# Optimization experiments

Hardware: AMD Instinct MI355X
Metric: run time of the kernel (lower is better)

The kernel has to match this reference:

```python
import jax, jax.numpy as jnp
import numpy as np

B, T, F, U, M = 4096, 16, 256, 512, 8
DELTA_T = 0.04

# ln_tau_table: tau = 1, 10^0.5, 10^1.0, ... -> ln(tau) = i * 0.5*ln(10)
LN_TAU = (jnp.arange(M, dtype=jnp.float32) * (0.5 * np.log(10.0))).astype(jnp.float32)
DECAY = jnp.exp(-DELTA_T / (LN_TAU + 1e-7))  # [M]


def setup_inputs() -> dict:
    key = jax.random.key(0)
    ks = jax.random.split(key, 9)
    s = lambda fan_in: 1.0 / np.sqrt(fan_in)
    return {
        "x": jax.random.normal(ks[0], (B, T, F), dtype=jnp.float32),
        "W_r": jax.random.normal(ks[1], (F + U, U * M), dtype=jnp.float32) * s(F + U),
        "b_r": jax.random.normal(ks[2], (U * M,), dtype=jnp.float32) * 0.01,
        "W_q": jax.random.normal(ks[3], (F + U, U), dtype=jnp.float32) * s(F + U),
        "b_q": jax.random.normal(ks[4], (U,), dtype=jnp.float32) * 0.01,
        "W_s": jax.random.normal(ks[5], (F + U, U * M), dtype=jnp.float32) * s(F + U),
        "b_s": jax.random.normal(ks[6], (U * M,), dtype=jnp.float32) * 0.01,
        "W_out": jax.random.normal(ks[7], (U, 3), dtype=jnp.float32) * s(U),
        "b_out": jax.random.normal(ks[8], (3,), dtype=jnp.float32) * 0.01,
    }


def _ctgru_forward(x, W_r, b_r, W_q, b_q, W_s, b_s, W_out, b_out):
    def step(h_hat, x_t):  # h_hat: [B,U,M], x_t: [B,F]
        h = h_hat.sum(axis=2)                              # [B,U]
        fused = jnp.concatenate([x_t, h], axis=1)          # [B,F+U]
        ln_tau_r = (fused @ W_r + b_r).reshape(-1, U, M)   # [B,U,M]
        r_ki = jax.nn.softmax(-jnp.square(ln_tau_r - LN_TAU), axis=2)
        q_in = jnp.concatenate([x_t, jnp.sum(r_ki * h_hat, axis=2)], axis=1)
        q_k = jnp.tanh(q_in @ W_q + b_q)[:, :, None]       # [B,U,1]
        ln_tau_s = (fused @ W_s + b_s).reshape(-1, U, M)
        s_ki = jax.nn.softmax(-jnp.square(ln_tau_s - LN_TAU), axis=2)
        h_next = ((1.0 - s_ki) * h_hat + s_ki * q_k) * DECAY
        return h_next, h_next.sum(axis=2)                  # carry, hidden [B,U]

    h0 = jnp.zeros((x.shape[0], U, M), dtype=x.dtype)
    _, hiddens = jax.lax.scan(step, h0, jnp.swapaxes(x, 0, 1))  # hiddens: [T,B,U]
    outputs = jnp.swapaxes(hiddens, 0, 1)                  # [B,T,U]
    return outputs @ W_out + b_out                         # [B,T,3]


def reference(x, W_r, b_r, W_q, b_q, W_s, b_s, W_out, b_out):
    return _ctgru_forward(x, W_r, b_r, W_q, b_q, W_s, b_s, W_out, b_out)
```

## Files before the change

### kernel.cpp

```cpp
#include <hip/hip_runtime.h>
#include <hip/hip_bf16.h>
#include <math.h>

#define B_   4096
#define T_   16
#define F_   256
#define U_   512
#define M_   8
#define K_   768
#define NRS  4096
#define NC   8192
#define LNT  1.1512925f

typedef __bf16 bf16_t;
typedef bf16_t bf16x8 __attribute__((ext_vector_type(8)));
typedef bf16_t bf16x4 __attribute__((ext_vector_type(4)));
typedef float  f32x4  __attribute__((ext_vector_type(4)));

__device__ inline void gl_lds16(const void* g, void* lds) {
    __builtin_amdgcn_global_load_lds(
        (const __attribute__((address_space(1))) unsigned int*)g,
        (__attribute__((address_space(3))) unsigned int*)lds, 16, 0, 0);
}

#define VMCNT(n) asm volatile("s_waitcnt vmcnt(" #n ")" ::: "memory")
#define LGKM0()  asm volatile("s_waitcnt lgkmcnt(0)" ::: "memory")
#define BAR()    __builtin_amdgcn_s_barrier()

__device__ inline void stage_slot(const bf16_t* src, bf16_t* dst, int tid) {
    gl_lds16(src + tid * 8,        (char*)dst + tid * 16);
    gl_lds16(src + tid * 8 + 4096, (char*)dst + tid * 16 + 8192);
}

__device__ inline void ds_read4(const bf16_t* base, bf16x8 (&v)[4]) {
    v[0] = *(const bf16x8*)(base);
    v[1] = *(const bf16x8*)(base + 512);
    v[2] = *(const bf16x8*)(base + 1024);
    v[3] = *(const bf16x8*)(base + 1536);
}

template <int H>
__device__ inline void mfma16(f32x4 (&acc)[8][4], const bf16x8 (&a)[4],
                              const bf16x8 (&b)[4]) {
    __builtin_amdgcn_s_setprio(1);
#pragma unroll
    for (int i = 0; i < 4; ++i)
#pragma unroll
        for (int j = 0; j < 4; ++j)
            acc[H * 4 + i][j] = __builtin_amdgcn_mfma_f32_16x16x32_bf16(
                a[i], b[j], acc[H * 4 + i][j], 0, 0, 0);
    __builtin_amdgcn_s_setprio(0);
}

__global__ __launch_bounds__(512, 2) void gemm_rs_tp(
    const bf16_t* __restrict__ xt_t,
    const bf16_t* __restrict__ ht,
    const bf16_t* __restrict__ Bt,
    const float*  __restrict__ biasP,
    const bf16_t* __restrict__ hhat,
    bf16_t* __restrict__ rh,
    bf16_t* __restrict__ sbuf)
{
    __shared__ __attribute__((aligned(16))) bf16_t Asl[2][8192];
    __shared__ __attribute__((aligned(16))) bf16_t Bsl[2][8192];

    const int tid  = threadIdx.x;
    const int lane = tid & 63;
    const int wave = tid >> 6;

    const int lin = blockIdx.y * 16 + blockIdx.x;
    const int xcd = lin & 7, q = lin >> 3;
    const int m0 = ((xcd >> 1) * 4 + (q & 3)) * 256;
    const int n0 = ((xcd & 1) * 16 + (q >> 2)) * 256;
    const int mp = m0 >> 8, np = n0 >> 8;

    const int wm = wave >> 2;
    const int wn = wave & 3;
    const int lr = lane & 15;
    const int kq = lane >> 4;
    const int cr = (kq ^ ((lr >> 1) & 3)) * 8;

    const int aoff0 = (wm * 128 + lr) * 32 + cr;
    const int aoff1 = (wm * 128 + 64 + lr) * 32 + cr;
    const int boff  = (wn * 64 + lr) * 32 + cr;

    f32x4 acc[8][4] = {};
    bf16x8 a[4], b[4];

#define ASRC(S) ((S) < 8 ? xt_t + (size_t)(mp * 8 + (S)) * 8192               \
                         : ht   + (size_t)(mp * 16 + (S) - 8) * 8192)
#define BSRC(S) (Bt + (size_t)(np * 24 + (S)) * 8192)

    stage_slot(ASRC(0), &Asl[0][0], tid);
    stage_slot(BSRC(0), &Bsl[0][0], tid);
    VMCNT(0);
    BAR();

#define TILE(T, SFLAG)                                                        \
  {                                                                           \
    const int p_ = (T) & 1, pn_ = p_ ^ 1;                                     \
    if (SFLAG) {                                                              \
      stage_slot(ASRC((T) + 1), &Asl[pn_][0], tid);                           \
      stage_slot(BSRC((T) + 1), &Bsl[pn_][0], tid);                           \
    }                                                                         \
    ds_read4(&Asl[p_][0] + aoff0, a);                                         \
    ds_read4(&Bsl[p_][0] + boff, b);                                          \
    LGKM0();                                                                  \
    mfma16<0>(acc, a, b);                                                     \
    ds_read4(&Asl[p_][0] + aoff1, a);                                         \
    LGKM0();                                                                  \
    mfma16<1>(acc, a, b);                                                     \
    VMCNT(0);                                                                 \
    BAR();                                                                    \
  }

    for (int tt = 0; tt < 22; tt += 2) { TILE(tt, 1); TILE(tt + 1, 1); }
    TILE(22, 1);
    TILE(23, 0);
#undef TILE
#undef ASRC
#undef BSRC

    const int nb  = n0 + wn * 64;
    const int u3  = lane & 7;
    const int m0v = ((lane >> 3) & 1) * 4;
    const bool is_r = nb < NRS;

    float bj[4];
#pragma unroll
    for (int j = 0; j < 4; ++j) bj[j] = biasP[nb + j * 16 + lr];

#pragma unroll
    for (int mi = 0; mi < 8; ++mi) {
        const int rowb = m0 + wm * 128 + mi * 16 + kq * 4;
#pragma unroll
        for (int r = 0; r < 4; ++r) {
            const int row = rowb + r;
            float e[4], sum = 0.f;
#pragma unroll
            for (int j = 0; j < 4; ++j) {
                float v = acc[mi][j][r] + bj[j];
                float d = v - (float)(m0v + j) * LNT;
                e[j] = __expf(-d * d);
                sum += e[j];
            }
            sum += __shfl_xor(sum, 8, 64);
            const float inv = 1.0f / sum;
            if (is_r) {
                bf16x4 h4 = *(const bf16x4*)(hhat + (size_t)row * NRS + nb + u3 * 8 + m0v);
                float rhv = 0.f;
#pragma unroll
                for (int j = 0; j < 4; ++j) rhv += e[j] * inv * (float)h4[j];
                rhv += __shfl_xor(rhv, 8, 64);
                if ((lane & 8) == 0)
                    rh[(size_t)row * U_ + (nb >> 3) + u3] = (bf16_t)rhv;
            } else {
                bf16x4 pv;
#pragma unroll
                for (int j = 0; j < 4; ++j) pv[j] = (bf16_t)(e[j] * inv);
                *(bf16x4*)(sbuf + (size_t)row * NRS + (nb - NRS) + u3 * 8 + m0v) = pv;
            }
        }
    }
}

__global__ __launch_bounds__(256) void gemm_q_up(
    const bf16_t* __restrict__ xt_t,
    const bf16_t* __restrict__ rh,
    const bf16_t* __restrict__ Bq,
    const float*  __restrict__ bq,
    const bf16_t* __restrict__ sbuf,
    bf16_t* __restrict__ hhat,
    bf16_t* __restrict__ hnext,
    bf16_t* __restrict__ htile)
{
    __shared__ __attribute__((aligned(16))) bf16_t Al[2][64 * 32];
    __shared__ __attribute__((aligned(16))) bf16_t Bl[2][64 * 32];

    const int tid  = threadIdx.x;
    const int lane = tid & 63;
    const int wave = tid >> 6;
    const int m0 = blockIdx.x * 64;
    const int n0 = blockIdx.y * 64;
    const int wm = (wave & 1) * 32;
    const int wn = (wave >> 1) * 32;
    const int lr = lane & 15;
    const int kq = lane >> 4;
    const int crq = (kq ^ ((lr >> 1) & 3)) * 8;

    f32x4 acc[2][2] = {};

    const int rA  = tid >> 2;
    const int kc  = (tid & 3) * 8;
    const int kcs = ((tid & 3) ^ ((tid >> 3) & 3)) * 8;

    for (int kk = 0; kk < K_; kk += 64) {
        __syncthreads();
        if (kk < F_) {
            const bf16_t* s0p = xt_t + (size_t)((m0 >> 8) * 8 + (kk >> 5)) * 8192
                                     + (size_t)(m0 & 255) * 32;
            gl_lds16(s0p + tid * 8,        (char*)&Al[0][0] + tid * 16);
            gl_lds16(s0p + 8192 + tid * 8, (char*)&Al[1][0] + tid * 16);
        } else {
            const int cb = kk - F_;
            gl_lds16(rh + (size_t)(m0 + rA) * U_ + cb + kcs,      (char*)&Al[0][0] + tid * 16);
            gl_lds16(rh + (size_t)(m0 + rA) * U_ + cb + 32 + kcs, (char*)&Al[1][0] + tid * 16);
        }
        gl_lds16(Bq + (size_t)(n0 + rA) * K_ + kk + kc,      (char*)&Bl[0][0] + tid * 16);
        gl_lds16(Bq + (size_t)(n0 + rA) * K_ + kk + 32 + kc, (char*)&Bl[1][0] + tid * 16);
        __syncthreads();

#pragma unroll
        for (int s = 0; s < 2; s++) {
            bf16x8 af[2], bfr[2];
#pragma unroll
            for (int i = 0; i < 2; i++)
                af[i] = *(const bf16x8*)(&Al[s][0] + (wm + i * 16 + lr) * 32 + crq);
#pragma unroll
            for (int i = 0; i < 2; i++)
                bfr[i] = *(const bf16x8*)(&Bl[s][0] + (wn + i * 16 + lr) * 32 + kq * 8);
#pragma unroll
            for (int i = 0; i < 2; i++)
#pragma unroll
                for (int j = 0; j < 2; j++)
                    acc[i][j] = __builtin_amdgcn_mfma_f32_16x16x32_bf16(
                        af[i], bfr[j], acc[i][j], 0, 0, 0);
        }
    }

    const float DEC[8] = {0.0f, 0.9658531f, 0.9827783f, 0.9884856f,
                          0.9913518f, 0.9930754f, 0.9942261f, 0.9950489f};

#pragma unroll
    for (int i = 0; i < 2; i++) {
        const int rowb = m0 + wm + i * 16 + kq * 4;
#pragma unroll
        for (int j = 0; j < 2; j++) {
            const int u = n0 + wn + j * 16 + lr;
            const float bv = bq[u];
            const int us = u >> 5, uc = u & 31;
#pragma unroll
            for (int r = 0; r < 4; r++) {
                const int row = rowb + r;
                const float q = tanhf(acc[i][j][r] + bv);
                const size_t base = (size_t)row * NRS + u * 8;
                bf16x8 s8 = *(const bf16x8*)(sbuf + base);
                bf16x8 h8 = *(const bf16x8*)(hhat + base);
                bf16x8 ho;
                float hs = 0.f;
#pragma unroll
                for (int m = 0; m < 8; m++) {
                    float s = (float)s8[m];
                    float h = (float)h8[m];
                    float hn = ((1.f - s) * h + s * q) * DEC[m];
                    ho[m] = (bf16_t)hn;
                    hs += hn;
                }
                *(bf16x8*)(hhat + base) = ho;
                hnext[(size_t)row * U_ + u] = (bf16_t)hs;
                const int rl = row & 255;
                htile[(size_t)((row >> 8) * 16 + us) * 8192 + rl * 32
                      + (((uc >> 3) ^ ((rl >> 1) & 3)) * 8) + (uc & 7)] = (bf16_t)hs;
            }
        }
    }
}

__global__ void transpose_perm(const float* __restrict__ src, bf16_t* __restrict__ dst) {
    __shared__ float tl[32][33];
    int k0 = blockIdx.x * 32, n0 = blockIdx.y * 32;
    int tx = threadIdx.x & 31, ty = threadIdx.x >> 5;
#pragma unroll
    for (int i = 0; i < 32; i += 8)
        tl[ty + i][tx] = src[(size_t)(k0 + ty + i) * NRS + n0 + tx];
    __syncthreads();
#pragma unroll
    for (int i = 0; i < 32; i += 8) {
        int n = n0 + ty + i;
        int m = n & 7, u3v = (n >> 3) & 7;
        int p = (n & ~63) + (m & 3) * 16 + (m >> 2) * 8 + u3v;
        dst[(size_t)p * K_ + k0 + tx] = (bf16_t)tl[tx][ty + i];
    }
}

__global__ void btile_build(const bf16_t* __restrict__ WrsT, bf16_t* __restrict__ Bt) {
    int n = blockIdx.x / 3;
    int k = (blockIdx.x % 3) * 256 + threadIdx.x;
    int p = n >> 8, r = n & 255, s = k >> 5, c = k & 31;
    Bt[(size_t)(p * 24 + s) * 8192 + r * 32
       + (((c >> 3) ^ ((r >> 1) & 3)) * 8) + (c & 7)] = WrsT[(size_t)n * K_ + k];
}

__global__ void transpose_plain(const float* __restrict__ src, bf16_t* __restrict__ dst, int N) {
    __shared__ float tl[32][33];
    int k0 = blockIdx.x * 32, n0 = blockIdx.y * 32;
    int tx = threadIdx.x & 31, ty = threadIdx.x >> 5;
#pragma unroll
    for (int i = 0; i < 32; i += 8)
        tl[ty + i][tx] = src[(size_t)(k0 + ty + i) * N + n0 + tx];
    __syncthreads();
#pragma unroll
    for (int i = 0; i < 32; i += 8)
        dst[(size_t)(n0 + ty + i) * K_ + k0 + tx] = (bf16_t)tl[tx][ty + i];
}

__global__ void bias_perm(const float* __restrict__ b_r, const float* __restrict__ b_s,
                          float* __restrict__ biasP) {
    int p = blockIdx.x * 256 + threadIdx.x;
    int pr = p & 63, j = pr >> 4, lr = pr & 15;
    int L = (p & ~63) + (lr & 7) * 8 + ((lr >> 3) & 1) * 4 + j;
    biasP[p] = (L < NRS) ? b_r[L] : b_s[L - NRS];
}

__global__ void xtile_build(const float* __restrict__ x, bf16_t* __restrict__ xt) {
    int idx = blockIdx.x * 256 + threadIdx.x;
    int b = idx >> 12;
    int rem = idx & 4095;
    int t = rem >> 8, f = rem & 255;
    int mp = b >> 8, r = b & 255, s = f >> 5, c = f & 31;
    xt[((size_t)(t * 16 + mp) * 8 + s) * 8192 + r * 32
       + (((c >> 3) ^ ((r >> 1) & 3)) * 8) + (c & 7)] = (bf16_t)x[idx];
}

__global__ __launch_bounds__(256) void out_all(
    const bf16_t* __restrict__ hall,
    const float* __restrict__ Wout,
    const float* __restrict__ bout,
    float* __restrict__ out)
{
    int row = blockIdx.x * 4 + (threadIdx.x >> 6);
    int lane = threadIdx.x & 63;
    bf16x8 h8 = *(const bf16x8*)(hall + (size_t)row * U_ + lane * 8);
    float p0 = 0, p1 = 0, p2 = 0;
#pragma unroll
    for (int k = 0; k < 8; k++) {
        float h = (float)h8[k];
        int u = lane * 8 + k;
        p0 += h * Wout[u * 3 + 0];
        p1 += h * Wout[u * 3 + 1];
        p2 += h * Wout[u * 3 + 2];
    }
    for (int off = 32; off; off >>= 1) {
        p0 += __shfl_down(p0, off, 64);
        p1 += __shfl_down(p1, off, 64);
        p2 += __shfl_down(p2, off, 64);
    }
    if (lane == 0) {
        int t = row >> 12, b = row & (B_ - 1);
        size_t o = ((size_t)b * T_ + t) * 3;
        out[o + 0] = p0 + bout[0];
        out[o + 1] = p1 + bout[1];
        out[o + 2] = p2 + bout[2];
    }
}

extern "C" void kernel_launch(void* const* d_in, const int* in_sizes, int n_in,
                              void* d_out, int out_size, void* d_ws, size_t ws_size,
                              hipStream_t stream) {
    const float* x   = (const float*)d_in[0];
    const float* W_r = (const float*)d_in[1];
    const float* b_r = (const float*)d_in[2];
    const float* W_q = (const float*)d_in[3];
    const float* b_q = (const float*)d_in[4];
    const float* W_s = (const float*)d_in[5];
    const float* b_s = (const float*)d_in[6];
    const float* W_o = (const float*)d_in[7];
    const float* b_o = (const float*)d_in[8];
    float* out = (float*)d_out;

    char* ws = (char*)d_ws;
    bf16_t* hhat  = (bf16_t*)ws; ws += (size_t)B_ * NRS * 2;
    bf16_t* sbuf  = (bf16_t*)ws; ws += (size_t)B_ * NRS * 2;
    bf16_t* xtile = (bf16_t*)ws; ws += (size_t)B_ * T_ * F_ * 2;
    bf16_t* hall  = (bf16_t*)ws; ws += (size_t)(T_ + 1) * B_ * U_ * 2;
    bf16_t* rh    = (bf16_t*)ws; ws += (size_t)B_ * U_ * 2;
    bf16_t* WrsT  = (bf16_t*)ws; ws += (size_t)NC * K_ * 2;
    bf16_t* Btile = (bf16_t*)ws; ws += (size_t)NC * K_ * 2;
    bf16_t* htile = (bf16_t*)ws; ws += (size_t)B_ * U_ * 2;
    bf16_t* WqT   = (bf16_t*)ws; ws += (size_t)U_ * K_ * 2;
    float*  biasP = (float*)ws;  ws += (size_t)NC * 4;

    hipMemsetAsync(hhat, 0, (size_t)B_ * NRS * 2, stream);
    hipMemsetAsync(htile, 0, (size_t)B_ * U_ * 2, stream);
    xtile_build<<<B_ * T_ * F_ / 256, 256, 0, stream>>>(x, xtile);
    transpose_perm<<<dim3(K_ / 32, NRS / 32), 256, 0, stream>>>(W_r, WrsT);
    transpose_perm<<<dim3(K_ / 32, NRS / 32), 256, 0, stream>>>(W_s, WrsT + (size_t)NRS * K_);
    btile_build<<<NC * 3, 256, 0, stream>>>(WrsT, Btile);
    transpose_plain<<<dim3(K_ / 32, U_ / 32), 256, 0, stream>>>(W_q, WqT, U_);
    bias_perm<<<NC / 256, 256, 0, stream>>>(b_r, b_s, biasP);

    for (int t = 0; t < T_; t++) {
        const bf16_t* xt_t = xtile + (size_t)t * 16 * 8 * 8192;
        bf16_t*       hn   = hall + (size_t)(t + 1) * B_ * U_;
        gemm_rs_tp<<<dim3(16, 32), 512, 0, stream>>>(xt_t, htile, Btile, biasP, hhat, rh, sbuf);
        gemm_q_up<<<dim3(64, 8), 256, 0, stream>>>(xt_t, rh, WqT, b_q, sbuf, hhat, hn, htile);
    }
    out_all<<<B_ * T_ / 4, 256, 0, stream>>>(hall + (size_t)B_ * U_, W_o, b_o, out);
}
```

Before: 1.792 ms.

## Restructure rs GEMM to K=64 tiles with 8-phase interleaved LDS pipeline

The main r/s GEMM now stages 64-wide K tiles split into halves and double-buffers them across two slots. Each iteration runs an 8-phase schedule that interleaves LDS reads, global-to-LDS loads and MFMA quarters, with barriers between phases. The swizzled tile layouts for x, h, W_rs and a new pre-tiled W_q are rewritten to a 64-column XOR swizzle, so the q GEMM can load B directly from tiles. LDS use rises to 128KB, so occupancy drops to one block per CU, and the many barriers add sync cost in exchange for better overlap of loads with MFMA.

```diff
diff --git a/kernel.cpp b/kernel.cpp
--- a/kernel.cpp
+++ b/kernel.cpp
@@ -27,32 +27,12 @@
 #define LGKM0()  asm volatile("s_waitcnt lgkmcnt(0)" ::: "memory")
 #define BAR()    __builtin_amdgcn_s_barrier()
 
-__device__ inline void stage_slot(const bf16_t* src, bf16_t* dst, int tid) {
+__device__ inline void stage_ht(const bf16_t* src, bf16_t* dst, int tid) {
     gl_lds16(src + tid * 8,        (char*)dst + tid * 16);
     gl_lds16(src + tid * 8 + 4096, (char*)dst + tid * 16 + 8192);
 }
 
-__device__ inline void ds_read4(const bf16_t* base, bf16x8 (&v)[4]) {
-    v[0] = *(const bf16x8*)(base);
-    v[1] = *(const bf16x8*)(base + 512);
-    v[2] = *(const bf16x8*)(base + 1024);
-    v[3] = *(const bf16x8*)(base + 1536);
-}
-
-template <int H>
-__device__ inline void mfma16(f32x4 (&acc)[8][4], const bf16x8 (&a)[4],
-                              const bf16x8 (&b)[4]) {
-    __builtin_amdgcn_s_setprio(1);
-#pragma unroll
-    for (int i = 0; i < 4; ++i)
-#pragma unroll
-        for (int j = 0; j < 4; ++j)
-            acc[H * 4 + i][j] = __builtin_amdgcn_mfma_f32_16x16x32_bf16(
-                a[i], b[j], acc[H * 4 + i][j], 0, 0, 0);
-    __builtin_amdgcn_s_setprio(0);
-}
-
-__global__ __launch_bounds__(512, 2) void gemm_rs_tp(
+__global__ __launch_bounds__(512, 1) void gemm_rs_v8(
     const bf16_t* __restrict__ xt_t,
     const bf16_t* __restrict__ ht,
     const bf16_t* __restrict__ Bt,
@@ -61,8 +41,8 @@
     bf16_t* __restrict__ rh,
     bf16_t* __restrict__ sbuf)
 {
-    __shared__ __attribute__((aligned(16))) bf16_t Asl[2][8192];
-    __shared__ __attribute__((aligned(16))) bf16_t Bsl[2][8192];
+    __shared__ __attribute__((aligned(16))) bf16_t Ah[2][2][8192];
+    __shared__ __attribute__((aligned(16))) bf16_t Bh[2][2][8192];
 
     const int tid  = threadIdx.x;
     const int lane = tid & 63;
@@ -78,57 +58,107 @@
     const int wn = wave & 3;
     const int lr = lane & 15;
     const int kq = lane >> 4;
-    const int cr = (kq ^ ((lr >> 1) & 3)) * 8;
-
-    const int aoff0 = (wm * 128 + lr) * 32 + cr;
-    const int aoff1 = (wm * 128 + 64 + lr) * 32 + cr;
-    const int boff  = (wn * 64 + lr) * 32 + cr;
+    const int ck0 = (kq ^ (lr & 7)) * 8;
+
+    const bf16_t* Ab0 = &Ah[0][wm][0] + lr * 64;
+    const bf16_t* Ab1 = &Ah[1][wm][0] + lr * 64;
+    const bf16_t* Bb0 = &Bh[0][wn >> 1][0] + ((wn & 1) * 64 + lr) * 64;
+    const bf16_t* Bb1 = &Bh[1][wn >> 1][0] + ((wn & 1) * 64 + lr) * 64;
 
     f32x4 acc[8][4] = {};
-    bf16x8 a[4], b[4];
-
-#define ASRC(S) ((S) < 8 ? xt_t + (size_t)(mp * 8 + (S)) * 8192               \
-                         : ht   + (size_t)(mp * 16 + (S) - 8) * 8192)
-#define BSRC(S) (Bt + (size_t)(np * 24 + (S)) * 8192)
-
-    stage_slot(ASRC(0), &Asl[0][0], tid);
-    stage_slot(BSRC(0), &Bsl[0][0], tid);
-    VMCNT(0);
+    bf16x8 a[8], b[8];
+
+#define AS(T, H) ((T) < 4 ? xt_t + ((size_t)(mp * 4 + (T)) * 2 + (H)) * 8192  \
+                          : ht  + ((size_t)(mp * 8 + (T) - 4) * 2 + (H)) * 8192)
+#define BS(T, H) (Bt + ((size_t)(np * 12 + (T)) * 2 + (H)) * 8192)
+
+#define RDA(P, mh) do{ const bf16_t* _p = (P) + (mh) * 4096;                   \
+    a[0]=*(const bf16x8*)(_p+ck0);      a[1]=*(const bf16x8*)(_p+(ck0^32));    \
+    a[2]=*(const bf16x8*)(_p+1024+ck0); a[3]=*(const bf16x8*)(_p+1024+(ck0^32)); \
+    a[4]=*(const bf16x8*)(_p+2048+ck0); a[5]=*(const bf16x8*)(_p+2048+(ck0^32)); \
+    a[6]=*(const bf16x8*)(_p+3072+ck0); a[7]=*(const bf16x8*)(_p+3072+(ck0^32)); }while(0)
+
+#define RDB(P, nh) do{ const bf16_t* _p = (P) + (nh) * 2048;                   \
+    b[(nh)*4+0]=*(const bf16x8*)(_p+ck0);                                      \
+    b[(nh)*4+1]=*(const bf16x8*)(_p+(ck0^32));                                 \
+    b[(nh)*4+2]=*(const bf16x8*)(_p+1024+ck0);                                 \
+    b[(nh)*4+3]=*(const bf16x8*)(_p+1024+(ck0^32)); }while(0)
+
+#define MMA(MH, NH) do{ __builtin_amdgcn_s_setprio(1);                         \
+    _Pragma("unroll") for (int ai = 0; ai < 4; ++ai)                           \
+      _Pragma("unroll") for (int bj = 0; bj < 2; ++bj)                         \
+        acc[(MH)*4+ai][(NH)*2+bj] = __builtin_amdgcn_mfma_f32_16x16x32_bf16(   \
+            a[ai*2+0], b[(NH)*4+bj*2+0], acc[(MH)*4+ai][(NH)*2+bj], 0, 0, 0);  \
+    _Pragma("unroll") for (int ai = 0; ai < 4; ++ai)                           \
+      _Pragma("unroll") for (int bj = 0; bj < 2; ++bj)                         \
+        acc[(MH)*4+ai][(NH)*2+bj] = __builtin_amdgcn_mfma_f32_16x16x32_bf16(   \
+            a[ai*2+1], b[(NH)*4+bj*2+1], acc[(MH)*4+ai][(NH)*2+bj], 0, 0, 0);  \
+    __builtin_amdgcn_s_setprio(0); }while(0)
+
+    stage_ht(AS(0, 0), &Ah[0][0][0], tid);
+    stage_ht(AS(0, 1), &Ah[0][1][0], tid);
+    stage_ht(BS(0, 0), &Bh[0][0][0], tid);
+    stage_ht(BS(0, 1), &Bh[0][1][0], tid);
+    stage_ht(AS(1, 0), &Ah[1][0][0], tid);
+    stage_ht(AS(1, 1), &Ah[1][1][0], tid);
+    stage_ht(BS(1, 0), &Bh[1][0][0], tid);
+    stage_ht(BS(1, 1), &Bh[1][1][0], tid);
+    VMCNT(8);
     BAR();
 
-#define TILE(T, SFLAG)                                                        \
-  {                                                                           \
-    const int p_ = (T) & 1, pn_ = p_ ^ 1;                                     \
-    if (SFLAG) {                                                              \
-      stage_slot(ASRC((T) + 1), &Asl[pn_][0], tid);                           \
-      stage_slot(BSRC((T) + 1), &Bsl[pn_][0], tid);                           \
-    }                                                                         \
-    ds_read4(&Asl[p_][0] + aoff0, a);                                         \
-    ds_read4(&Bsl[p_][0] + boff, b);                                          \
-    LGKM0();                                                                  \
-    mfma16<0>(acc, a, b);                                                     \
-    ds_read4(&Asl[p_][0] + aoff1, a);                                         \
-    LGKM0();                                                                  \
-    mfma16<1>(acc, a, b);                                                     \
-    VMCNT(0);                                                                 \
-    BAR();                                                                    \
-  }
-
-    for (int tt = 0; tt < 22; tt += 2) { TILE(tt, 1); TILE(tt + 1, 1); }
-    TILE(22, 1);
-    TILE(23, 0);
-#undef TILE
-#undef ASRC
-#undef BSRC
+#define ITER_S(E) do{                                                          \
+    RDA(Ab0,0); RDB(Bb0,0);                    BAR(); LGKM0(); MMA(0,0); BAR();\
+    RDB(Bb0,1);                                BAR(); LGKM0(); MMA(0,1); BAR();\
+    RDA(Ab0,1); stage_ht(BS((E)+2,0), &Bh[0][0][0], tid);                      \
+                                               BAR(); LGKM0(); MMA(1,1); BAR();\
+    stage_ht(BS((E)+2,1), &Bh[0][1][0], tid);                                  \
+                                    BAR(); LGKM0(); MMA(1,0); VMCNT(4); BAR(); \
+    RDA(Ab1,0); RDB(Bb1,0); stage_ht(AS((E)+2,0), &Ah[0][0][0], tid);          \
+                                               BAR(); LGKM0(); MMA(0,0); BAR();\
+    RDB(Bb1,1); stage_ht(AS((E)+2,1), &Ah[0][1][0], tid);                      \
+                                               BAR(); LGKM0(); MMA(0,1); BAR();\
+    RDA(Ab1,1); stage_ht(BS((E)+3,0), &Bh[1][0][0], tid);                      \
+                                               BAR(); LGKM0(); MMA(1,1); BAR();\
+    stage_ht(BS((E)+3,1), &Bh[1][1][0], tid);                                  \
+    stage_ht(AS((E)+3,0), &Ah[1][0][0], tid);                                  \
+    stage_ht(AS((E)+3,1), &Ah[1][1][0], tid);                                  \
+                                    BAR(); LGKM0(); MMA(1,0); VMCNT(8); BAR(); \
+}while(0)
+
+#define ITER_L() do{                                                           \
+    RDA(Ab0,0); RDB(Bb0,0);                    BAR(); LGKM0(); MMA(0,0); BAR();\
+    RDB(Bb0,1);                                BAR(); LGKM0(); MMA(0,1); BAR();\
+    RDA(Ab0,1);                                BAR(); LGKM0(); MMA(1,1); BAR();\
+                                    BAR(); LGKM0(); MMA(1,0); VMCNT(0); BAR(); \
+    RDA(Ab1,0); RDB(Bb1,0);                    BAR(); LGKM0(); MMA(0,0); BAR();\
+    RDB(Bb1,1);                                BAR(); LGKM0(); MMA(0,1); BAR();\
+    RDA(Ab1,1);                                BAR(); LGKM0(); MMA(1,1); BAR();\
+                                               BAR(); LGKM0(); MMA(1,0);       \
+}while(0)
+
+    ITER_S(0);
+    ITER_S(2);
+    ITER_S(4);
+    ITER_S(6);
+    ITER_S(8);
+    ITER_L();
+
+#undef ITER_S
+#undef ITER_L
+#undef MMA
+#undef RDA
+#undef RDB
+#undef AS
+#undef BS
 
     const int nb  = n0 + wn * 64;
     const int u3  = lane & 7;
     const int m0v = ((lane >> 3) & 1) * 4;
     const bool is_r = nb < NRS;
 
-    float bj[4];
-#pragma unroll
-    for (int j = 0; j < 4; ++j) bj[j] = biasP[nb + j * 16 + lr];
+    float bj4[4];
+#pragma unroll
+    for (int j = 0; j < 4; ++j) bj4[j] = biasP[nb + j * 16 + lr];
 
 #pragma unroll
     for (int mi = 0; mi < 8; ++mi) {
@@ -139,7 +169,7 @@
             float e[4], sum = 0.f;
 #pragma unroll
             for (int j = 0; j < 4; ++j) {
-                float v = acc[mi][j][r] + bj[j];
+                float v = acc[mi][j][r] + bj4[j];
                 float d = v - (float)(m0v + j) * LNT;
                 e[j] = __expf(-d * d);
                 sum += e[j];
@@ -167,65 +197,70 @@
 __global__ __launch_bounds__(256) void gemm_q_up(
     const bf16_t* __restrict__ xt_t,
     const bf16_t* __restrict__ rh,
-    const bf16_t* __restrict__ Bq,
+    const bf16_t* __restrict__ Bqt,
     const float*  __restrict__ bq,
     const bf16_t* __restrict__ sbuf,
     bf16_t* __restrict__ hhat,
     bf16_t* __restrict__ hnext,
     bf16_t* __restrict__ htile)
 {
-    __shared__ __attribute__((aligned(16))) bf16_t Al[2][64 * 32];
-    __shared__ __attribute__((aligned(16))) bf16_t Bl[2][64 * 32];
+    __shared__ __attribute__((aligned(16))) bf16_t As[4096];
+    __shared__ __attribute__((aligned(16))) bf16_t Bs[4096];
 
     const int tid  = threadIdx.x;
     const int lane = tid & 63;
     const int wave = tid >> 6;
     const int m0 = blockIdx.x * 64;
     const int n0 = blockIdx.y * 64;
-    const int wm = (wave & 1) * 32;
-    const int wn = (wave >> 1) * 32;
+    const int wm = wave & 1;
+    const int wn = wave >> 1;
     const int lr = lane & 15;
     const int kq = lane >> 4;
-    const int crq = (kq ^ ((lr >> 1) & 3)) * 8;
+    const int ck0 = (kq ^ (lr & 7)) * 8;
+
+    const int mp = m0 >> 8, half = (m0 >> 7) & 1, r0 = m0 & 127;
+    const int rw = tid >> 3, q8 = tid & 7;
 
     f32x4 acc[2][2] = {};
 
-    const int rA  = tid >> 2;
-    const int kc  = (tid & 3) * 8;
-    const int kcs = ((tid & 3) ^ ((tid >> 3) & 3)) * 8;
-
-    for (int kk = 0; kk < K_; kk += 64) {
+    for (int kt = 0; kt < 12; ++kt) {
         __syncthreads();
-        if (kk < F_) {
-            const bf16_t* s0p = xt_t + (size_t)((m0 >> 8) * 8 + (kk >> 5)) * 8192
-                                     + (size_t)(m0 & 255) * 32;
-            gl_lds16(s0p + tid * 8,        (char*)&Al[0][0] + tid * 16);
-            gl_lds16(s0p + 8192 + tid * 8, (char*)&Al[1][0] + tid * 16);
+        if (kt < 4) {
+            const bf16_t* s = xt_t + ((size_t)(mp * 4 + kt) * 2 + half) * 8192 + r0 * 64;
+            gl_lds16(s + tid * 8,        (char*)As + tid * 16);
+            gl_lds16(s + tid * 8 + 2048, (char*)As + tid * 16 + 4096);
         } else {
-            const int cb = kk - F_;
-            gl_lds16(rh + (size_t)(m0 + rA) * U_ + cb + kcs,      (char*)&Al[0][0] + tid * 16);
-            gl_lds16(rh + (size_t)(m0 + rA) * U_ + cb + 32 + kcs, (char*)&Al[1][0] + tid * 16);
+            const int cb = (kt - 4) * 64;
+            gl_lds16(rh + (size_t)(m0 + rw) * U_ + cb + ((q8 ^ (rw & 7)) * 8),
+                     (char*)As + tid * 16);
+            gl_lds16(rh + (size_t)(m0 + 32 + rw) * U_ + cb + ((q8 ^ (rw & 7)) * 8),
+                     (char*)As + tid * 16 + 4096);
         }
-        gl_lds16(Bq + (size_t)(n0 + rA) * K_ + kk + kc,      (char*)&Bl[0][0] + tid * 16);
-        gl_lds16(Bq + (size_t)(n0 + rA) * K_ + kk + 32 + kc, (char*)&Bl[1][0] + tid * 16);
+        {
+            const bf16_t* s = Bqt + (size_t)((n0 >> 6) * 12 + kt) * 4096;
+            gl_lds16(s + tid * 8,        (char*)Bs + tid * 16);
+            gl_lds16(s + tid * 8 + 2048, (char*)Bs + tid * 16 + 4096);
+        }
         __syncthreads();
 
-#pragma unroll
-        for (int s = 0; s < 2; s++) {
-            bf16x8 af[2], bfr[2];
-#pragma unroll
-            for (int i = 0; i < 2; i++)
-                af[i] = *(const bf16x8*)(&Al[s][0] + (wm + i * 16 + lr) * 32 + crq);
-#pragma unroll
-            for (int i = 0; i < 2; i++)
-                bfr[i] = *(const bf16x8*)(&Bl[s][0] + (wn + i * 16 + lr) * 32 + kq * 8);
+        bf16x8 af[4], bfr[4];
+#pragma unroll
+        for (int i = 0; i < 2; i++) {
+            const bf16_t* pa = As + (wm * 32 + i * 16 + lr) * 64;
+            const bf16_t* pb = Bs + (wn * 32 + i * 16 + lr) * 64;
+            af[i * 2 + 0]  = *(const bf16x8*)(pa + ck0);
+            af[i * 2 + 1]  = *(const bf16x8*)(pa + (ck0 ^ 32));
+            bfr[i * 2 + 0] = *(const bf16x8*)(pb + ck0);
+            bfr[i * 2 + 1] = *(const bf16x8*)(pb + (ck0 ^ 32));
+        }
+#pragma unroll
+        for (int ks = 0; ks < 2; ks++)
 #pragma unroll
             for (int i = 0; i < 2; i++)
 #pragma unroll
                 for (int j = 0; j < 2; j++)
                     acc[i][j] = __builtin_amdgcn_mfma_f32_16x16x32_bf16(
-                        af[i], bfr[j], acc[i][j], 0, 0, 0);
-        }
+                        af[i * 2 + ks], bfr[j * 2 + ks], acc[i][j], 0, 0, 0);
     }
 
     const float DEC[8] = {0.0f, 0.9658531f, 0.9827783f, 0.9884856f,
@@ -233,16 +268,16 @@
 
 #pragma unroll
     for (int i = 0; i < 2; i++) {
-        const int rowb = m0 + wm + i * 16 + kq * 4;
+        const int rowb = m0 + wm * 32 + i * 16 + kq * 4;
 #pragma unroll
         for (int j = 0; j < 2; j++) {
-            const int u = n0 + wn + j * 16 + lr;
+            const int u = n0 + wn * 32 + j * 16 + lr;
             const float bv = bq[u];
-            const int us = u >> 5, uc = u & 31;
+            const int kt2 = u >> 6, kc = u & 63;
 #pragma unroll
             for (int r = 0; r < 4; r++) {
                 const int row = rowb + r;
-                const float q = tanhf(acc[i][j][r] + bv);
+                const float qv = tanhf(acc[i][j][r] + bv);
                 const size_t base = (size_t)row * NRS + u * 8;
                 bf16x8 s8 = *(const bf16x8*)(sbuf + base);
                 bf16x8 h8 = *(const bf16x8*)(hhat + base);
@@ -252,15 +287,15 @@
                 for (int m = 0; m < 8; m++) {
                     float s = (float)s8[m];
                     float h = (float)h8[m];
-                    float hn = ((1.f - s) * h + s * q) * DEC[m];
+                    float hn = ((1.f - s) * h + s * qv) * DEC[m];
                     ho[m] = (bf16_t)hn;
                     hs += hn;
                 }
                 *(bf16x8*)(hhat + base) = ho;
                 hnext[(size_t)row * U_ + u] = (bf16_t)hs;
-                const int rl = row & 255;
-                htile[(size_t)((row >> 8) * 16 + us) * 8192 + rl * 32
-                      + (((uc >> 3) ^ ((rl >> 1) & 3)) * 8) + (uc & 7)] = (bf16_t)hs;
+                htile[((((size_t)(row >> 8) * 8 + kt2) * 2 + ((row >> 7) & 1)) * 128
+                       + (row & 127)) * 64
+                      + (((kc >> 3) ^ (row & 7)) * 8) + (kc & 7)] = (bf16_t)hs;
             }
         }
     }
@@ -286,9 +321,10 @@
 __global__ void btile_build(const bf16_t* __restrict__ WrsT, bf16_t* __restrict__ Bt) {
     int n = blockIdx.x / 3;
     int k = (blockIdx.x % 3) * 256 + threadIdx.x;
-    int p = n >> 8, r = n & 255, s = k >> 5, c = k & 31;
-    Bt[(size_t)(p * 24 + s) * 8192 + r * 32
-       + (((c >> 3) ^ ((r >> 1) & 3)) * 8) + (c & 7)] = WrsT[(size_t)n * K_ + k];
+    int np = n >> 8, rp = n & 255, hf = rp >> 7, r = rp & 127;
+    int kt = k >> 6, kc = k & 63;
+    Bt[((((size_t)np * 12 + kt) * 2 + hf) * 128 + r) * 64
+       + (((kc >> 3) ^ (r & 7)) * 8) + (kc & 7)] = WrsT[(size_t)n * K_ + k];
 }
 
 __global__ void transpose_plain(const float* __restrict__ src, bf16_t* __restrict__ dst, int N) {
@@ -302,6 +338,15 @@
 #pragma unroll
     for (int i = 0; i < 32; i += 8)
         dst[(size_t)(n0 + ty + i) * K_ + k0 + tx] = (bf16_t)tl[tx][ty + i];
+}
+
+__global__ void bqtile_build(const bf16_t* __restrict__ WqT, bf16_t* __restrict__ Bqt) {
+    int n = blockIdx.x / 3;
+    int k = (blockIdx.x % 3) * 256 + threadIdx.x;
+    int np = n >> 6, r = n & 63;
+    int kt = k >> 6, kc = k & 63;
+    Bqt[(((size_t)np * 12 + kt) * 64 + r) * 64
+        + (((kc >> 3) ^ (r & 7)) * 8) + (kc & 7)] = WqT[(size_t)n * K_ + k];
 }
 
 __global__ void bias_perm(const float* __restrict__ b_r, const float* __restrict__ b_s,
@@ -317,9 +362,10 @@
     int b = idx >> 12;
     int rem = idx & 4095;
     int t = rem >> 8, f = rem & 255;
-    int mp = b >> 8, r = b & 255, s = f >> 5, c = f & 31;
-    xt[((size_t)(t * 16 + mp) * 8 + s) * 8192 + r * 32
-       + (((c >> 3) ^ ((r >> 1) & 3)) * 8) + (c & 7)] = (bf16_t)x[idx];
+    int mp = b >> 8, rp = b & 255, hf = rp >> 7, r = rp & 127;
+    int kt = f >> 6, kc = f & 63;
+    xt[(((((size_t)t * 16 + mp) * 4 + kt) * 2 + hf) * 128 + r) * 64
+       + (((kc >> 3) ^ (r & 7)) * 8) + (kc & 7)] = (bf16_t)x[idx];
 }
 
 __global__ __launch_bounds__(256) void out_all(
@@ -378,6 +424,7 @@
     bf16_t* Btile = (bf16_t*)ws; ws += (size_t)NC * K_ * 2;
     bf16_t* htile = (bf16_t*)ws; ws += (size_t)B_ * U_ * 2;
     bf16_t* WqT   = (bf16_t*)ws; ws += (size_t)U_ * K_ * 2;
+    bf16_t* Bqtil = (bf16_t*)ws; ws += (size_t)U_ * K_ * 2;
     float*  biasP = (float*)ws;  ws += (size_t)NC * 4;
 
     hipMemsetAsync(hhat, 0, (size_t)B_ * NRS * 2, stream);
@@ -387,13 +434,14 @@
     transpose_perm<<<dim3(K_ / 32, NRS / 32), 256, 0, stream>>>(W_s, WrsT + (size_t)NRS * K_);
     btile_build<<<NC * 3, 256, 0, stream>>>(WrsT, Btile);
     transpose_plain<<<dim3(K_ / 32, U_ / 32), 256, 0, stream>>>(W_q, WqT, U_);
+    bqtile_build<<<U_ * 3, 256, 0, stream>>>(WqT, Bqtil);
     bias_perm<<<NC / 256, 256, 0, stream>>>(b_r, b_s, biasP);
 
     for (int t = 0; t < T_; t++) {
-        const bf16_t* xt_t = xtile + (size_t)t * 16 * 8 * 8192;
+        const bf16_t* xt_t = xtile + (size_t)t * 16 * 4 * 2 * 8192;
         bf16_t*       hn   = hall + (size_t)(t + 1) * B_ * U_;
-        gemm_rs_tp<<<dim3(16, 32), 512, 0, stream>>>(xt_t, htile, Btile, biasP, hhat, rh, sbuf);
-        gemm_q_up<<<dim3(64, 8), 256, 0, stream>>>(xt_t, rh, WqT, b_q, sbuf, hhat, hn, htile);
+        gemm_rs_v8<<<dim3(16, 32), 512, 0, stream>>>(xt_t, htile, Btile, biasP, hhat, rh, sbuf);
+        gemm_q_up<<<dim3(64, 8), 256, 0, stream>>>(xt_t, rh, Bqtil, b_q, sbuf, hhat, hn, htile);
     }
     out_all<<<B_ * T_ / 4, 256, 0, stream>>>(hall + (size_t)B_ * U_, W_o, b_o, out);
 }
```

New measurement: 1.819 ms. No clear change (+1.5%).
